# Kernel tuning notes

Measured on AMD Instinct MI355X. Metric: run time of the kernel, lower is better.

Reference implementation:

```python
import jax, jax.numpy as jnp
import numpy as np

TEMP = 0.05
EPS_SUM = 1e-6
EPS_LOG = 1e-6

B, D, M, C = 512, 256, 131072, 2000


def setup_inputs() -> dict:
    key = jax.random.key(0)
    k1, k2, k3, k4 = jax.random.split(key, 4)
    results = jax.random.normal(k1, (B, D), dtype=jnp.float32)
    indexes = jax.random.randint(k2, (B,), 0, M, dtype=jnp.int64)
    # memory bank is L2-normalized in practice (_update_feature normalizes)
    feats = jax.random.normal(k3, (M, D), dtype=jnp.float32)
    feats = feats / jnp.maximum(jnp.linalg.norm(feats, axis=1, keepdims=True), 1e-12)
    labels = jax.random.randint(k4, (M,), 0, C, dtype=jnp.int64)
    return {"results": results, "indexes": indexes, "features": feats,
            "labels": labels, "num_clusters": C}


def reference(results, indexes, features, labels, num_clusters):
    # L2 normalize inputs (F.normalize, p=2, dim=1)
    inputs = results / jnp.maximum(jnp.linalg.norm(results, axis=1, keepdims=True), 1e-12)
    # HM forward: similarity against memory bank, scaled by temperature
    sims = jnp.einsum('bd,md->bm', inputs, features) / TEMP  # [B, M]
    # segment-sum over memory slots grouped by cluster label (index_add_)
    sim_c = jax.ops.segment_sum(sims.T, labels, num_segments=num_clusters)  # [C, B]
    counts = jax.ops.segment_sum(jnp.ones((features.shape[0],), dtype=sims.dtype),
                                 labels, num_segments=num_clusters)  # [C]
    mask = counts > 0  # [C]
    denom = jnp.where(mask, counts, 1.0)[:, None]
    vec = (sim_c / denom).T  # [B, C] cluster-averaged similarities
    # masked softmax over clusters (matches original: exp then mask then normalize)
    exps = jnp.exp(vec) * mask[None, :].astype(vec.dtype)
    probs = exps / (jnp.sum(exps, axis=1, keepdims=True) + EPS_SUM)
    # NLL loss with targets = labels[indexes]
    targets = labels[indexes]  # [B]
    logp = jnp.log(probs + EPS_LOG)
    picked = jnp.take_along_axis(logp, targets[:, None], axis=1)[:, 0]
    return -jnp.mean(picked)
```

## Files before the change

kernel.cpp:

```cpp
#include <hip/hip_runtime.h>
#include <hip/hip_bf16.h>

#define TEMP_F   0.05f
#define B_       512
#define D_       256
#define M_       131072
#define C_       2000
#define CAP      256
#define CSTRIDE  16

typedef __attribute__((ext_vector_type(8))) short bf16x8;
typedef __attribute__((ext_vector_type(4))) float f32x4;
typedef __attribute__((ext_vector_type(4))) unsigned short u16x4;

__device__ __forceinline__ unsigned short f2bf(float x) {
    __hip_bfloat16 h = __float2bfloat16(x);
    return *reinterpret_cast<unsigned short*>(&h);
}

__device__ __forceinline__ float block_reduce_sum256(float v, float* smem) {
    __syncthreads();
    #pragma unroll
    for (int off = 32; off >= 1; off >>= 1) v += __shfl_xor(v, off, 64);
    int wave = threadIdx.x >> 6;
    if ((threadIdx.x & 63) == 0) smem[wave] = v;
    __syncthreads();
    return smem[0] + smem[1] + smem[2] + smem[3];
}

__global__ __launch_bounds__(256) void scatter_cast_kernel(
        const int* __restrict__ labels, int* __restrict__ cursor,
        int* __restrict__ member,
        const float* __restrict__ results, unsigned short* __restrict__ inp) {
    int t = threadIdx.x, blk = blockIdx.x;
    int m = blk * 256 + t;
    int c = labels[m];
    int pos = atomicAdd(&cursor[c * CSTRIDE], 1);
    if (pos < CAP) member[c * CAP + pos] = m;
    inp[blk * 256 + t] = f2bf(results[blk * 256 + t]);
}

__global__ __launch_bounds__(256) void centroid_kernel(
        const float* __restrict__ features, const int* __restrict__ cursor,
        const int* __restrict__ member, unsigned short* __restrict__ cs,
        float* __restrict__ maskf) {
    __shared__ int mlist[CAP];
    __shared__ f32x4 part[4][64];
    int c = blockIdx.x, t = threadIdx.x;
    int n = cursor[c * CSTRIDE];
    int nn = min(n, CAP);
    if (t < nn) mlist[t] = member[c * CAP + t];
    __syncthreads();
    int w = t >> 6;
    int l = t & 63;
    f32x4 a0 = {0.f, 0.f, 0.f, 0.f}, a1 = {0.f, 0.f, 0.f, 0.f};
    int i = w;
    for (; i + 4 < nn; i += 8) {
        f32x4 v0 = *reinterpret_cast<const f32x4*>(&features[(size_t)mlist[i] * D_ + l * 4]);
        f32x4 v1 = *reinterpret_cast<const f32x4*>(&features[(size_t)mlist[i + 4] * D_ + l * 4]);
        a0 += v0;
        a1 += v1;
    }
    if (i < nn)
        a0 += *reinterpret_cast<const f32x4*>(&features[(size_t)mlist[i] * D_ + l * 4]);
    part[w][l] = a0 + a1;
    __syncthreads();
    if (t < 64) {
        f32x4 s = part[0][t] + part[1][t] + part[2][t] + part[3][t];
        float scale = 1.0f / (TEMP_F * (float)max(n, 1));
        u16x4 o;
        o[0] = f2bf(s[0] * scale);
        o[1] = f2bf(s[1] * scale);
        o[2] = f2bf(s[2] * scale);
        o[3] = f2bf(s[3] * scale);
        *reinterpret_cast<u16x4*>(&cs[c * D_ + t * 4]) = o;
    }
    if (t == 0) maskf[c] = (n > 0) ? 1.0f : 0.0f;
}

__global__ __launch_bounds__(256) void gemm_kernel(
        const unsigned short* __restrict__ inp, const unsigned short* __restrict__ cs,
        float* __restrict__ vec) {
    int wave = threadIdx.x >> 6;
    int lane = threadIdx.x & 63;
    int tile = blockIdx.x * 4 + wave;
    int tb = tile / 125;
    int tc = tile - tb * 125;
    int row = lane & 15;
    int kg  = lane >> 4;
    const unsigned short* ap = inp + (size_t)(tb * 16 + row) * D_ + kg * 8;
    const unsigned short* bp = cs  + (size_t)(tc * 16 + row) * D_ + kg * 8;
    f32x4 acc = {0.f, 0.f, 0.f, 0.f};
    #pragma unroll
    for (int k0 = 0; k0 < D_; k0 += 32) {
        bf16x8 a = *reinterpret_cast<const bf16x8*>(ap + k0);
        bf16x8 b = *reinterpret_cast<const bf16x8*>(bp + k0);
        acc = __builtin_amdgcn_mfma_f32_16x16x32_bf16(a, b, acc, 0, 0, 0);
    }
    int ccol  = tc * 16 + (lane & 15);
    int brow0 = tb * 16 + kg * 4;
    #pragma unroll
    for (int r = 0; r < 4; ++r)
        vec[(size_t)(brow0 + r) * C_ + ccol] = acc[r];
}

__global__ __launch_bounds__(256) void loss_kernel(
        const float* __restrict__ results, const float* __restrict__ vec,
        const float* __restrict__ maskf, const int* __restrict__ labels,
        const int* __restrict__ indexes, float* __restrict__ out) {
    __shared__ float smem[4];
    int b = blockIdx.x, t = threadIdx.x;
    float rv = results[b * D_ + t];
    float nrm2 = block_reduce_sum256(rv * rv, smem);
    float inv = 1.0f / fmaxf(sqrtf(nrm2), 1e-12f);
    const f32x4* v4 = reinterpret_cast<const f32x4*>(&vec[(size_t)b * C_]);
    const f32x4* m4 = reinterpret_cast<const f32x4*>(maskf);
    float s = 0.f;
    for (int j = t; j < C_ / 4; j += 256) {
        f32x4 v = v4[j];
        f32x4 mk = m4[j];
        s += mk[0] * __expf(v[0] * inv) + mk[1] * __expf(v[1] * inv)
           + mk[2] * __expf(v[2] * inv) + mk[3] * __expf(v[3] * inv);
    }
    float S = block_reduce_sum256(s, smem);
    if (t == 0) {
        int tgt = labels[indexes[b]];
        float pt = __expf(vec[(size_t)b * C_ + tgt] * inv) / (S + 1e-6f);
        atomicAdd(out, -logf(pt + 1e-6f) * (1.0f / (float)B_));
    }
}

extern "C" void kernel_launch(void* const* d_in, const int* in_sizes, int n_in,
                              void* d_out, int out_size, void* d_ws, size_t ws_size,
                              hipStream_t stream) {
    const float* results  = (const float*)d_in[0];
    const int*   indexes  = (const int*)d_in[1];
    const float* features = (const float*)d_in[2];
    const int*   labels   = (const int*)d_in[3];
    float* out = (float*)d_out;

    char* w = (char*)d_ws;
    unsigned short* inp   = (unsigned short*)(w);
    int*            curs  = (int*)(w + 262144);
    int*            memb  = (int*)(w + 393216);
    unsigned short* cs    = (unsigned short*)(w + 2490368);
    float*          maskf = (float*)(w + 3538944);
    float*          vec   = (float*)(w + 3547136);

    hipMemsetAsync(curs, 0, C_ * CSTRIDE * sizeof(int), stream);
    hipMemsetAsync(out, 0, sizeof(float), stream);
    scatter_cast_kernel<<<M_ / 256, 256, 0, stream>>>(labels, curs, memb, results, inp);
    centroid_kernel<<<C_, 256, 0, stream>>>(features, curs, memb, cs, maskf);
    gemm_kernel<<<1000, 256, 0, stream>>>(inp, cs, vec);
    loss_kernel<<<B_, 256, 0, stream>>>(results, vec, maskf, labels, indexes, out);
}
```

Baseline: 234.7 us.

## Fuse cluster GEMM with softmax-NLL loss and widen centroid gather unroll

Merges the bf16 MFMA similarity GEMM and the loss kernel into one kernel. Each block handles 16 batch rows, keeps its A fragments in registers, and reduces exp-sums and the target logit on the fly. This removes the [B,C] fp32 vec buffer write and re-read and one kernel launch. The centroid gather now uses four independent accumulators for more memory-level parallelism. The trade-off is that the fused kernel launches only 32 blocks, so most CUs sit idle during the GEMM phase.

Result: slower. 261.9 us (+11.6%).

```diff
diff --git a/kernel.cpp b/kernel.cpp
--- a/kernel.cpp
+++ b/kernel.cpp
@@ -16,16 +16,6 @@
 __device__ __forceinline__ unsigned short f2bf(float x) {
     __hip_bfloat16 h = __float2bfloat16(x);
     return *reinterpret_cast<unsigned short*>(&h);
-}
-
-__device__ __forceinline__ float block_reduce_sum256(float v, float* smem) {
-    __syncthreads();
-    #pragma unroll
-    for (int off = 32; off >= 1; off >>= 1) v += __shfl_xor(v, off, 64);
-    int wave = threadIdx.x >> 6;
-    if ((threadIdx.x & 63) == 0) smem[wave] = v;
-    __syncthreads();
-    return smem[0] + smem[1] + smem[2] + smem[3];
 }
 
 __global__ __launch_bounds__(256) void scatter_cast_kernel(
@@ -53,17 +43,18 @@
     __syncthreads();
     int w = t >> 6;
     int l = t & 63;
-    f32x4 a0 = {0.f, 0.f, 0.f, 0.f}, a1 = {0.f, 0.f, 0.f, 0.f};
+    f32x4 a0 = {0.f,0.f,0.f,0.f}, a1 = {0.f,0.f,0.f,0.f};
+    f32x4 a2 = {0.f,0.f,0.f,0.f}, a3 = {0.f,0.f,0.f,0.f};
     int i = w;
-    for (; i + 4 < nn; i += 8) {
-        f32x4 v0 = *reinterpret_cast<const f32x4*>(&features[(size_t)mlist[i] * D_ + l * 4]);
-        f32x4 v1 = *reinterpret_cast<const f32x4*>(&features[(size_t)mlist[i + 4] * D_ + l * 4]);
-        a0 += v0;
-        a1 += v1;
+    for (; i + 12 < nn; i += 16) {
+        a0 += *reinterpret_cast<const f32x4*>(&features[(size_t)mlist[i     ] * D_ + l * 4]);
+        a1 += *reinterpret_cast<const f32x4*>(&features[(size_t)mlist[i +  4] * D_ + l * 4]);
+        a2 += *reinterpret_cast<const f32x4*>(&features[(size_t)mlist[i +  8] * D_ + l * 4]);
+        a3 += *reinterpret_cast<const f32x4*>(&features[(size_t)mlist[i + 12] * D_ + l * 4]);
     }
-    if (i < nn)
+    for (; i < nn; i += 4)
         a0 += *reinterpret_cast<const f32x4*>(&features[(size_t)mlist[i] * D_ + l * 4]);
-    part[w][l] = a0 + a1;
+    part[w][l] = (a0 + a1) + (a2 + a3);
     __syncthreads();
     if (t < 64) {
         f32x4 s = part[0][t] + part[1][t] + part[2][t] + part[3][t];
@@ -78,54 +69,76 @@
     if (t == 0) maskf[c] = (n > 0) ? 1.0f : 0.0f;
 }
 
-__global__ __launch_bounds__(256) void gemm_kernel(
+__global__ __launch_bounds__(256) void gemm_loss_kernel(
         const unsigned short* __restrict__ inp, const unsigned short* __restrict__ cs,
-        float* __restrict__ vec) {
-    int wave = threadIdx.x >> 6;
-    int lane = threadIdx.x & 63;
-    int tile = blockIdx.x * 4 + wave;
-    int tb = tile / 125;
-    int tc = tile - tb * 125;
-    int row = lane & 15;
-    int kg  = lane >> 4;
-    const unsigned short* ap = inp + (size_t)(tb * 16 + row) * D_ + kg * 8;
-    const unsigned short* bp = cs  + (size_t)(tc * 16 + row) * D_ + kg * 8;
-    f32x4 acc = {0.f, 0.f, 0.f, 0.f};
+        const float* __restrict__ results, const float* __restrict__ maskf,
+        const int* __restrict__ labels, const int* __restrict__ indexes,
+        float* __restrict__ out) {
+    __shared__ float inv[16];
+    __shared__ int   tgtc[16];
+    __shared__ float rowsum[4][16];
+    __shared__ float tgtlog[16];
+    int tb = blockIdx.x;
+    int t = threadIdx.x;
+    int wave = t >> 6, lane = t & 63;
+    {
+        int r = t >> 4, seg = t & 15;
+        const f32x4* rp = reinterpret_cast<const f32x4*>(
+            &results[(size_t)(tb * 16 + r) * D_ + seg * 16]);
+        float s = 0.f;
+        #pragma unroll
+        for (int q = 0; q < 4; ++q) {
+            f32x4 v = rp[q];
+            s += v[0]*v[0] + v[1]*v[1] + v[2]*v[2] + v[3]*v[3];
+        }
+        s += __shfl_xor(s, 1, 64);
+        s += __shfl_xor(s, 2, 64);
+        s += __shfl_xor(s, 4, 64);
+        s += __shfl_xor(s, 8, 64);
+        if (seg == 0) inv[r] = 1.0f / fmaxf(sqrtf(s), 1e-12f);
+        if (t < 16) tgtc[t] = labels[indexes[tb * 16 + t]];
+    }
+    __syncthreads();
+    int row16 = lane & 15, kg = lane >> 4;
+    float myinv[4];
+    int mytgt[4];
     #pragma unroll
-    for (int k0 = 0; k0 < D_; k0 += 32) {
-        bf16x8 a = *reinterpret_cast<const bf16x8*>(ap + k0);
-        bf16x8 b = *reinterpret_cast<const bf16x8*>(bp + k0);
-        acc = __builtin_amdgcn_mfma_f32_16x16x32_bf16(a, b, acc, 0, 0, 0);
+    for (int r = 0; r < 4; ++r) { myinv[r] = inv[kg*4 + r]; mytgt[r] = tgtc[kg*4 + r]; }
+    const unsigned short* ap = inp + (size_t)(tb * 16 + row16) * D_ + kg * 8;
+    bf16x8 afr[8];
+    #pragma unroll
+    for (int q = 0; q < 8; ++q) afr[q] = *reinterpret_cast<const bf16x8*>(ap + q * 32);
+    float ssum[4] = {0.f, 0.f, 0.f, 0.f};
+    for (int tc = wave; tc < C_ / 16; tc += 4) {
+        const unsigned short* bp = cs + (size_t)(tc * 16 + row16) * D_ + kg * 8;
+        f32x4 acc = {0.f, 0.f, 0.f, 0.f};
+        #pragma unroll
+        for (int q = 0; q < 8; ++q) {
+            bf16x8 b = *reinterpret_cast<const bf16x8*>(bp + q * 32);
+            acc = __builtin_amdgcn_mfma_f32_16x16x32_bf16(afr[q], b, acc, 0, 0, 0);
+        }
+        int col = tc * 16 + row16;
+        float mk = maskf[col];
+        #pragma unroll
+        for (int r = 0; r < 4; ++r) {
+            float lg = acc[r] * myinv[r];
+            ssum[r] += mk * __expf(lg);
+            if (col == mytgt[r]) tgtlog[kg*4 + r] = lg;
+        }
     }
-    int ccol  = tc * 16 + (lane & 15);
-    int brow0 = tb * 16 + kg * 4;
     #pragma unroll
-    for (int r = 0; r < 4; ++r)
-        vec[(size_t)(brow0 + r) * C_ + ccol] = acc[r];
-}
-
-__global__ __launch_bounds__(256) void loss_kernel(
-        const float* __restrict__ results, const float* __restrict__ vec,
-        const float* __restrict__ maskf, const int* __restrict__ labels,
-        const int* __restrict__ indexes, float* __restrict__ out) {
-    __shared__ float smem[4];
-    int b = blockIdx.x, t = threadIdx.x;
-    float rv = results[b * D_ + t];
-    float nrm2 = block_reduce_sum256(rv * rv, smem);
-    float inv = 1.0f / fmaxf(sqrtf(nrm2), 1e-12f);
-    const f32x4* v4 = reinterpret_cast<const f32x4*>(&vec[(size_t)b * C_]);
-    const f32x4* m4 = reinterpret_cast<const f32x4*>(maskf);
-    float s = 0.f;
-    for (int j = t; j < C_ / 4; j += 256) {
-        f32x4 v = v4[j];
-        f32x4 mk = m4[j];
-        s += mk[0] * __expf(v[0] * inv) + mk[1] * __expf(v[1] * inv)
-           + mk[2] * __expf(v[2] * inv) + mk[3] * __expf(v[3] * inv);
+    for (int r = 0; r < 4; ++r) {
+        float s = ssum[r];
+        s += __shfl_xor(s, 1, 64);
+        s += __shfl_xor(s, 2, 64);
+        s += __shfl_xor(s, 4, 64);
+        s += __shfl_xor(s, 8, 64);
+        if (row16 == 0) rowsum[wave][kg*4 + r] = s;
     }
-    float S = block_reduce_sum256(s, smem);
-    if (t == 0) {
-        int tgt = labels[indexes[b]];
-        float pt = __expf(vec[(size_t)b * C_ + tgt] * inv) / (S + 1e-6f);
+    __syncthreads();
+    if (t < 16) {
+        float S = rowsum[0][t] + rowsum[1][t] + rowsum[2][t] + rowsum[3][t];
+        float pt = __expf(tgtlog[t]) / (S + 1e-6f);
         atomicAdd(out, -logf(pt + 1e-6f) * (1.0f / (float)B_));
     }
 }
@@ -145,12 +158,10 @@
     int*            memb  = (int*)(w + 393216);
     unsigned short* cs    = (unsigned short*)(w + 2490368);
     float*          maskf = (float*)(w + 3538944);
-    float*          vec   = (float*)(w + 3547136);
 
     hipMemsetAsync(curs, 0, C_ * CSTRIDE * sizeof(int), stream);
     hipMemsetAsync(out, 0, sizeof(float), stream);
     scatter_cast_kernel<<<M_ / 256, 256, 0, stream>>>(labels, curs, memb, results, inp);
     centroid_kernel<<<C_, 256, 0, stream>>>(features, curs, memb, cs, maskf);
-    gemm_kernel<<<1000, 256, 0, stream>>>(inp, cs, vec);
-    loss_kernel<<<B_, 256, 0, stream>>>(results, vec, maskf, labels, indexes, out);
+    gemm_loss_kernel<<<B_ / 16, 256, 0, stream>>>(inp, cs, results, maskf, labels, indexes, out);
 }
```
